# Kernel tuning notes

Measured on AMD Instinct MI355X. Metric: run time of the kernel, lower is better.

## Reference

```python
import jax, jax.numpy as jnp
import numpy as np

NUM_HEADS = 16
THETA = 10000.0
B, S, D = 2, 2048, 1024
D_K = D // NUM_HEADS


def setup_inputs() -> dict:
    key = jax.random.key(0)
    ks = jax.random.split(key, 5)
    s = 0.02
    return {
        "x": jax.random.normal(ks[0], (B, S, D), dtype=jnp.float32),
        "W_q": jax.random.normal(ks[1], (D, D), dtype=jnp.float32) * s,
        "W_k": jax.random.normal(ks[2], (D, D), dtype=jnp.float32) * s,
        "W_v": jax.random.normal(ks[3], (D, D), dtype=jnp.float32) * s,
        "W_o": jax.random.normal(ks[4], (D, D), dtype=jnp.float32) * s,
        "token_positions": jnp.arange(S, dtype=jnp.int32),
    }


def _rope(x, token_positions):
    # x: [..., seq, d_k]; equivalent to the block-diagonal 2x2 rotation matmul
    d2 = x.shape[-1] // 2
    inv_freq = THETA ** (-(2.0 * jnp.arange(d2, dtype=x.dtype)) / x.shape[-1])  # [d2]
    ang = token_positions.astype(x.dtype)[:, None] * inv_freq[None, :]  # [seq, d2]
    cos, sin = jnp.cos(ang), jnp.sin(ang)
    xp = x.reshape(x.shape[:-1] + (d2, 2))
    xe, xo = xp[..., 0], xp[..., 1]
    oe = cos * xe - sin * xo
    oo = sin * xe + cos * xo
    return jnp.stack([oe, oo], axis=-1).reshape(x.shape)


def reference(x, W_q, W_k, W_v, W_o, token_positions):
    seq = x.shape[-2]
    # QKV projections (weights stored as [out, in])
    Q = jnp.einsum('bsd,ed->bse', x, W_q)
    K = jnp.einsum('bsd,ed->bse', x, W_k)
    V = jnp.einsum('bsd,ed->bse', x, W_v)
    def split_heads(t):
        return t.reshape(t.shape[:-1] + (NUM_HEADS, D_K)).swapaxes(-3, -2)  # [b,h,s,dk]
    Q, K, V = split_heads(Q), split_heads(K), split_heads(V)
    Q = _rope(Q, token_positions)
    K = _rope(K, token_positions)
    scale = 1.0 / np.sqrt(D_K)
    scores = jnp.einsum('bhqd,bhkd->bhqk', Q, K) * scale
    causal = jnp.tril(jnp.ones((seq, seq), dtype=bool))
    scores = jnp.where(causal, scores, -jnp.inf)
    probs = jax.nn.softmax(scores, axis=-1)
    out = jnp.einsum('bhqk,bhkd->bhqd', probs, V)
    out = out.swapaxes(-3, -2).reshape(x.shape[:-1] + (D,))
    return jnp.einsum('bse,de->bsd', out, W_o)
```

## Files before the change

### kernel.cpp

```cpp
#include <hip/hip_runtime.h>
#include <hip/hip_bf16.h>
#include <math.h>

#define H_    16
#define DK_   64
#define Dm    1024
#define Bb    2
#define Ss    2048
#define Mrows 4096
#define QSCALE 0.1803368801f

typedef short s16x8 __attribute__((ext_vector_type(8)));
typedef float f32x4 __attribute__((ext_vector_type(4)));
typedef unsigned short u16;

__device__ __forceinline__ u16 f2b(float f) {
  __hip_bfloat16 h = __float2bfloat16(f);
  return *reinterpret_cast<u16*>(&h);
}
__device__ __forceinline__ float b2f(u16 u) {
  __hip_bfloat16 h;
  *reinterpret_cast<u16*>(&h) = u;
  return __bfloat162float(h);
}

#define GLDS(g, l)                                                             \
  __builtin_amdgcn_global_load_lds(                                            \
      (const __attribute__((address_space(1))) unsigned int*)(g),              \
      (__attribute__((address_space(3))) unsigned int*)(l), 16, 0, 0)

__device__ __forceinline__ int SW64(int row, int col) {
  return row * 64 + ((((col >> 3) ^ (row & 7) ^ (row >> 3)) & 7) << 3) + (col & 7);
}

__global__ __launch_bounds__(256) void k_castall(
    const float* __restrict__ x,  const float* __restrict__ Wq,
    const float* __restrict__ Wk, const float* __restrict__ Wv,
    const float* __restrict__ Wo,
    u16* __restrict__ xb,  u16* __restrict__ wqb, u16* __restrict__ wkb,
    u16* __restrict__ wvb, u16* __restrict__ wob) {
  int i = blockIdx.x * 256 + threadIdx.x;
  const float* s;
  u16* d;
  int off;
  if (i < 1048576) { s = x; d = xb; off = i; }
  else {
    int j = i - 1048576;
    int w = j >> 18;
    off = j & 262143;
    s = (w == 0) ? Wq : (w == 1) ? Wk : (w == 2) ? Wv : Wo;
    d = (w == 0) ? wqb : (w == 1) ? wkb : (w == 2) ? wvb : wob;
  }
  float4 v = reinterpret_cast<const float4*>(s)[off];
  ushort4 o;
  o.x = f2b(v.x); o.y = f2b(v.y); o.z = f2b(v.z); o.w = f2b(v.w);
  reinterpret_cast<ushort4*>(d)[off] = o;
}

__global__ __launch_bounds__(256) void k_ropetab(const int* __restrict__ pos,
                                                 float2* __restrict__ tab) {
  int t = blockIdx.x * 256 + threadIdx.x;
  int s = t >> 5, i = t & 31;
  float p = (float)pos[s];
  float ang = p * powf(10000.0f, -(float)i / 32.0f);
  tab[t] = make_float2(cosf(ang), sinf(ang));
}

__global__ __launch_bounds__(256) void k_rope2(u16* __restrict__ Q, u16* __restrict__ K,
                                               const float2* __restrict__ tab) {
  int t = blockIdx.x * 256 + threadIdx.x;
  int row = t >> 7;
  int c0 = (t & 127) << 3;
  int i0 = (c0 & 63) >> 1;
  const float2* tb = &tab[(row & (Ss - 1)) * 32 + i0];
  float2 cs[4];
#pragma unroll
  for (int j = 0; j < 4; ++j) cs[j] = tb[j];
  size_t off = (size_t)row * Dm + c0;
  s16x8 q = *reinterpret_cast<const s16x8*>(&Q[off]);
  s16x8 k = *reinterpret_cast<const s16x8*>(&K[off]);
  s16x8 qo, ko;
#pragma unroll
  for (int j = 0; j < 4; ++j) {
    float qe = b2f((u16)q[2 * j]), qd = b2f((u16)q[2 * j + 1]);
    qo[2 * j]     = (short)f2b((cs[j].x * qe - cs[j].y * qd) * QSCALE);
    qo[2 * j + 1] = (short)f2b((cs[j].y * qe + cs[j].x * qd) * QSCALE);
    float ke = b2f((u16)k[2 * j]), kd = b2f((u16)k[2 * j + 1]);
    ko[2 * j]     = (short)f2b(cs[j].x * ke - cs[j].y * kd);
    ko[2 * j + 1] = (short)f2b(cs[j].y * ke + cs[j].x * kd);
  }
  *reinterpret_cast<s16x8*>(&Q[off]) = qo;
  *reinterpret_cast<s16x8*>(&K[off]) = ko;
}

template <int BN>
__global__ __launch_bounds__(256) void k_gemm_bt(
    const u16* __restrict__ A,
    const u16* __restrict__ B0, const u16* __restrict__ B1, const u16* __restrict__ B2,
    u16* __restrict__ O0, u16* __restrict__ O1, u16* __restrict__ OVT,
    float* __restrict__ OF, int M, int N, int K, int f32out) {
  constexpr int NFR = BN / 32;
  __shared__ __align__(16) u16 lsA[128 * 32];
  __shared__ __align__(16) u16 lsB[BN * 32];
  const int tid = threadIdx.x, lane = tid & 63, wave = tid >> 6;
  const int quad = lane >> 4, l16 = lane & 15;
  const int wrow = wave >> 1, wcol = wave & 1;
  const int m0 = blockIdx.x * 128, n0 = blockIdx.y * BN;
  const int z = blockIdx.z;
  const u16* Bp = (z == 0) ? B0 : (z == 1) ? B1 : B2;
  u16* Op = (z == 0) ? O0 : O1;
  f32x4 acc[4][NFR] = {};

  for (int k0 = 0; k0 < K; k0 += 32) {
#pragma unroll
    for (int c = 0; c < 2; ++c) {
      int flat = (wave * 2 + c) * 512 + lane * 8;
      int row = flat >> 5;
      int gs = ((flat >> 3) & 3) ^ ((row >> 1) & 3);
      GLDS(A + (size_t)(m0 + row) * K + k0 + gs * 8, lsA + (wave * 2 + c) * 512);
    }
#pragma unroll
    for (int c = 0; c < BN / 64; ++c) {
      int cc = wave * (BN / 64) + c;
      int flat = cc * 512 + lane * 8;
      int row = flat >> 5;
      int gs = ((flat >> 3) & 3) ^ ((row >> 1) & 3);
      GLDS(Bp + (size_t)(n0 + row) * K + k0 + gs * 8, lsB + cc * 512);
    }
    __syncthreads();
    s16x8 af[4], bfr[NFR];
#pragma unroll
    for (int i = 0; i < 4; ++i) {
      int row = wrow * 64 + i * 16 + l16;
      af[i] = *reinterpret_cast<const s16x8*>(&lsA[row * 32 + ((quad ^ ((row >> 1) & 3)) << 3)]);
    }
#pragma unroll
    for (int i = 0; i < NFR; ++i) {
      int row = wcol * (BN / 2) + i * 16 + l16;
      bfr[i] = *reinterpret_cast<const s16x8*>(&lsB[row * 32 + ((quad ^ ((row >> 1) & 3)) << 3)]);
    }
#pragma unroll
    for (int mi = 0; mi < 4; ++mi)
#pragma unroll
      for (int ni = 0; ni < NFR; ++ni)
        acc[mi][ni] = __builtin_amdgcn_mfma_f32_16x16x32_bf16(af[mi], bfr[ni], acc[mi][ni], 0, 0, 0);
    __syncthreads();
  }

  if (!f32out && z == 2) {
#pragma unroll
    for (int mi = 0; mi < 4; ++mi)
#pragma unroll
      for (int ni = 0; ni < NFR; ++ni) {
        int row0 = m0 + wrow * 64 + mi * 16 + quad * 4;
        int col  = n0 + wcol * (BN / 2) + ni * 16 + l16;
        int bb = row0 >> 11, s0 = row0 & (Ss - 1);
        ushort4 pk;
        pk.x = f2b(acc[mi][ni][0]); pk.y = f2b(acc[mi][ni][1]);
        pk.z = f2b(acc[mi][ni][2]); pk.w = f2b(acc[mi][ni][3]);
        *reinterpret_cast<ushort4*>(&OVT[((size_t)bb * Dm + col) * Ss + s0]) = pk;
      }
    return;
  }
#pragma unroll
  for (int mi = 0; mi < 4; ++mi)
#pragma unroll
    for (int ni = 0; ni < NFR; ++ni)
#pragma unroll
      for (int r = 0; r < 4; ++r) {
        int row = m0 + wrow * 64 + mi * 16 + quad * 4 + r;
        int col = n0 + wcol * (BN / 2) + ni * 16 + l16;
        float v = acc[mi][ni][r];
        size_t idx = (size_t)row * N + col;
        if (f32out) OF[idx] = v;
        else        Op[idx] = f2b(v);
      }
}

__global__ __launch_bounds__(256) void k_flash(const u16* __restrict__ Q,
                                               const u16* __restrict__ K,
                                               const u16* __restrict__ VT,
                                               u16* __restrict__ O) {
  __shared__ __align__(16) u16 lsK[2][64 * 64];
  __shared__ __align__(16) u16 lsVT[2][64 * 64];
  __shared__ __align__(16) u16 lsP[4][32 * 64];
  const int tid = threadIdx.x, lane = tid & 63, wave = tid >> 6;
  const int quad = lane >> 4, l16 = lane & 15;
  const int bid = blockIdx.x;
  const int bh = bid & 31;
  const int h = bh & (H_ - 1), b = bh >> 4;
  const int g = bid >> 5, a = g & 7, bsel = g >> 3;
  const int qt = bsel ? (15 - a) : a;
  const int q0 = qt * 128;
  const int qbase = q0 + wave * 32;
  const int ktmax_w = (qbase + 31) >> 6;
  const int xorv = (l16 * 2) & 0xE;

  s16x8 qf[2][2];
#pragma unroll
  for (int s = 0; s < 2; ++s) {
    const size_t qoff = (size_t)(b * Ss + qbase + s * 16 + l16) * Dm + h * 64;
    qf[s][0] = *reinterpret_cast<const s16x8*>(&Q[qoff + quad * 8]);
    qf[s][1] = *reinterpret_cast<const s16x8*>(&Q[qoff + 32 + quad * 8]);
  }
  s16x8 ones;
#pragma unroll
  for (int j = 0; j < 8; ++j) ones[j] = (short)0x3F80;

  f32x4 ot[2][4] = {};
  f32x4 lAcc[2] = {};
  const int npairs = qt + 1;

  for (int pp = 0; pp < npairs; ++pp) {
    const int kt0 = pp * 2;
#pragma unroll
    for (int half = 0; half < 2; ++half) {
      const size_t kbase  = (size_t)(b * Ss + (kt0 + half) * 64) * Dm + h * 64;
      const size_t vtbase = ((size_t)b * Dm + h * 64) * Ss + (kt0 + half) * 64;
#pragma unroll
      for (int c = 0; c < 2; ++c) {
        int slot = (wave * 2 + c) * 64 + lane;
        int row = slot >> 3;
        int gg = ((slot & 7) ^ (row & 7) ^ (row >> 3)) & 7;
        GLDS(K  + kbase  + (size_t)row * Dm + gg * 8, lsK[half]  + (wave * 2 + c) * 512);
        GLDS(VT + vtbase + (size_t)row * Ss + gg * 8, lsVT[half] + (wave * 2 + c) * 512);
      }
    }
    __syncthreads();

#pragma unroll
    for (int half = 0; half < 2; ++half) {
      const int kt = kt0 + half;
      if (kt > ktmax_w) break;
      f32x4 st[2][4] = {};
#pragma unroll
      for (int kc = 0; kc < 2; ++kc)
#pragma unroll
        for (int ni = 0; ni < 4; ++ni) {
          s16x8 kf = *reinterpret_cast<const s16x8*>(
              &lsK[half][SW64(ni * 16 + l16, kc * 32 + quad * 8)]);
          st[0][ni] = __builtin_amdgcn_mfma_f32_16x16x32_bf16(kf, qf[0][kc], st[0][ni], 0, 0, 0);
          st[1][ni] = __builtin_amdgcn_mfma_f32_16x16x32_bf16(kf, qf[1][kc], st[1][ni], 0, 0, 0);
        }
      if (kt == ktmax_w) {
#pragma unroll
        for (int s = 0; s < 2; ++s) {
          int gq = qbase + s * 16 + l16;
#pragma unroll
          for (int ni = 0; ni < 4; ++ni)
#pragma unroll
            for (int r = 0; r < 4; ++r)
              if (kt * 64 + ni * 16 + quad * 4 + r > gq) st[s][ni][r] = -INFINITY;
        }
      }
#pragma unroll
      for (int s = 0; s < 2; ++s)
#pragma unroll
        for (int ni = 0; ni < 4; ++ni) {
          ushort4 pk;
          pk.x = f2b(exp2f(st[s][ni][0])); pk.y = f2b(exp2f(st[s][ni][1]));
          pk.z = f2b(exp2f(st[s][ni][2])); pk.w = f2b(exp2f(st[s][ni][3]));
          *reinterpret_cast<ushort4*>(
              &lsP[wave][(s * 16 + l16) * 64 + (((ni * 4 + quad) ^ xorv) << 2)]) = pk;
        }
#pragma unroll
      for (int kc = 0; kc < 2; ++kc) {
        s16x8 pf0 = *reinterpret_cast<const s16x8*>(
            &lsP[wave][l16 * 64 + (((kc * 8 + quad * 2) ^ xorv) << 2)]);
        s16x8 pf1 = *reinterpret_cast<const s16x8*>(
            &lsP[wave][(16 + l16) * 64 + (((kc * 8 + quad * 2) ^ xorv) << 2)]);
        lAcc[0] = __builtin_amdgcn_mfma_f32_16x16x32_bf16(ones, pf0, lAcc[0], 0, 0, 0);
        lAcc[1] = __builtin_amdgcn_mfma_f32_16x16x32_bf16(ones, pf1, lAcc[1], 0, 0, 0);
#pragma unroll
        for (int ni = 0; ni < 4; ++ni) {
          s16x8 vf = *reinterpret_cast<const s16x8*>(
              &lsVT[half][SW64(ni * 16 + l16, kc * 32 + quad * 8)]);
          ot[0][ni] = __builtin_amdgcn_mfma_f32_16x16x32_bf16(vf, pf0, ot[0][ni], 0, 0, 0);
          ot[1][ni] = __builtin_amdgcn_mfma_f32_16x16x32_bf16(vf, pf1, ot[1][ni], 0, 0, 0);
        }
      }
    }
    __syncthreads();
  }

#pragma unroll
  for (int s = 0; s < 2; ++s) {
    float inv = 1.0f / lAcc[s][0];
    const size_t obase = (size_t)(b * Ss + qbase + s * 16 + l16) * Dm + h * 64;
#pragma unroll
    for (int ni = 0; ni < 4; ++ni) {
      ushort4 pk;
      pk.x = f2b(ot[s][ni][0] * inv); pk.y = f2b(ot[s][ni][1] * inv);
      pk.z = f2b(ot[s][ni][2] * inv); pk.w = f2b(ot[s][ni][3] * inv);
      *reinterpret_cast<ushort4*>(&O[obase + ni * 16 + quad * 4]) = pk;
    }
  }
}

extern "C" void kernel_launch(void* const* d_in, const int* in_sizes, int n_in,
                              void* d_out, int out_size, void* d_ws, size_t ws_size,
                              hipStream_t stream) {
  const float* x  = (const float*)d_in[0];
  const float* Wq = (const float*)d_in[1];
  const float* Wk = (const float*)d_in[2];
  const float* Wv = (const float*)d_in[3];
  const float* Wo = (const float*)d_in[4];
  const int* pos  = (const int*)d_in[5];
  float* out = (float*)d_out;

  char* w = (char*)d_ws;
  u16* xb  = (u16*)w; w += (size_t)Mrows * Dm * 2;
  u16* wqb = (u16*)w; w += (size_t)Dm * Dm * 2;
  u16* wkb = (u16*)w; w += (size_t)Dm * Dm * 2;
  u16* wvb = (u16*)w; w += (size_t)Dm * Dm * 2;
  u16* wob = (u16*)w; w += (size_t)Dm * Dm * 2;
  u16* Qb  = (u16*)w; w += (size_t)Mrows * Dm * 2;
  u16* Kb  = (u16*)w; w += (size_t)Mrows * Dm * 2;
  u16* VTb = (u16*)w; w += (size_t)Mrows * Dm * 2;
  u16* Ab  = (u16*)w; w += (size_t)Mrows * Dm * 2;
  float2* tabf = (float2*)w; w += (size_t)Ss * 32 * sizeof(float2);

  k_castall<<<8192, 256, 0, stream>>>(x, Wq, Wk, Wv, Wo, xb, wqb, wkb, wvb, wob);
  k_ropetab<<<Ss * 32 / 256, 256, 0, stream>>>(pos, tabf);

  k_gemm_bt<128><<<dim3(32, 8, 3), 256, 0, stream>>>(xb, wqb, wkb, wvb,
                                                     Qb, Kb, VTb, nullptr,
                                                     Mrows, Dm, Dm, 0);
  k_rope2<<<Mrows * Dm / 8 / 256, 256, 0, stream>>>(Qb, Kb, tabf);
  k_flash<<<dim3(512), 256, 0, stream>>>(Qb, Kb, VTb, Ab);
  k_gemm_bt<64><<<dim3(32, 16, 1), 256, 0, stream>>>(Ab, wob, wob, wob,
                                                     nullptr, nullptr, nullptr, out,
                                                     Mrows, Dm, Dm, 1);
}
```

Before: 203.1 us.

## Double-buffer flash K/V loads, widen GEMM k-step, use fast exp2 and pack

The flash kernel moves from loading pairs of K/V tiles and then computing on them to a per-tile double-buffered pipeline, where the next tile is prefetched while the current one is processed, with one barrier per tile. The projection GEMM now steps K by 64 with the SW64 swizzle, halving the number of barriers and loop iterations at the cost of larger LDS tiles. Softmax exponentials use the raw hardware exp2 builtin, and bf16 packing uses a byte-perm that truncates instead of rounding, trading a little precision for fewer instructions. There is a possible race: with one barrier per tile, a fast wave can issue the prefetch into a buffer that slower waves may still be reading from the previous iteration.

Measured after the change: 202.1 us. No clear change (-0.5%).

```diff
diff --git a/kernel.cpp b/kernel.cpp
--- a/kernel.cpp
+++ b/kernel.cpp
@@ -13,6 +13,7 @@
 typedef short s16x8 __attribute__((ext_vector_type(8)));
 typedef float f32x4 __attribute__((ext_vector_type(4)));
 typedef unsigned short u16;
+typedef unsigned int u32;
 
 __device__ __forceinline__ u16 f2b(float f) {
   __hip_bfloat16 h = __float2bfloat16(f);
@@ -22,6 +23,9 @@
   __hip_bfloat16 h;
   *reinterpret_cast<u16*>(&h) = u;
   return __bfloat162float(h);
+}
+__device__ __forceinline__ u32 pkbf(float hi, float lo) {
+  return __builtin_amdgcn_perm(__float_as_uint(hi), __float_as_uint(lo), 0x07060302u);
 }
 
 #define GLDS(g, l)                                                             \
@@ -100,8 +104,8 @@
     u16* __restrict__ O0, u16* __restrict__ O1, u16* __restrict__ OVT,
     float* __restrict__ OF, int M, int N, int K, int f32out) {
   constexpr int NFR = BN / 32;
-  __shared__ __align__(16) u16 lsA[128 * 32];
-  __shared__ __align__(16) u16 lsB[BN * 32];
+  __shared__ __align__(16) u16 lsA[128 * 64];
+  __shared__ __align__(16) u16 lsB[BN * 64];
   const int tid = threadIdx.x, lane = tid & 63, wave = tid >> 6;
   const int quad = lane >> 4, l16 = lane & 15;
   const int wrow = wave >> 1, wcol = wave & 1;
@@ -111,39 +115,38 @@
   u16* Op = (z == 0) ? O0 : O1;
   f32x4 acc[4][NFR] = {};
 
-  for (int k0 = 0; k0 < K; k0 += 32) {
-#pragma unroll
-    for (int c = 0; c < 2; ++c) {
-      int flat = (wave * 2 + c) * 512 + lane * 8;
-      int row = flat >> 5;
-      int gs = ((flat >> 3) & 3) ^ ((row >> 1) & 3);
-      GLDS(A + (size_t)(m0 + row) * K + k0 + gs * 8, lsA + (wave * 2 + c) * 512);
-    }
-#pragma unroll
-    for (int c = 0; c < BN / 64; ++c) {
-      int cc = wave * (BN / 64) + c;
-      int flat = cc * 512 + lane * 8;
-      int row = flat >> 5;
-      int gs = ((flat >> 3) & 3) ^ ((row >> 1) & 3);
-      GLDS(Bp + (size_t)(n0 + row) * K + k0 + gs * 8, lsB + cc * 512);
+  for (int k0 = 0; k0 < K; k0 += 64) {
+#pragma unroll
+    for (int c = 0; c < 4; ++c) {
+      int slot = (wave * 4 + c) * 64 + lane;
+      int row = slot >> 3;
+      int gg = ((slot & 7) ^ (row & 7) ^ (row >> 3)) & 7;
+      GLDS(A + (size_t)(m0 + row) * K + k0 + gg * 8, lsA + (wave * 4 + c) * 512);
+    }
+#pragma unroll
+    for (int c = 0; c < BN / 32; ++c) {
+      int cc = wave * (BN / 32) + c;
+      int slot = cc * 64 + lane;
+      int row = slot >> 3;
+      int gg = ((slot & 7) ^ (row & 7) ^ (row >> 3)) & 7;
+      GLDS(Bp + (size_t)(n0 + row) * K + k0 + gg * 8, lsB + cc * 512);
     }
     __syncthreads();
-    s16x8 af[4], bfr[NFR];
-#pragma unroll
-    for (int i = 0; i < 4; ++i) {
-      int row = wrow * 64 + i * 16 + l16;
-      af[i] = *reinterpret_cast<const s16x8*>(&lsA[row * 32 + ((quad ^ ((row >> 1) & 3)) << 3)]);
-    }
-#pragma unroll
-    for (int i = 0; i < NFR; ++i) {
-      int row = wcol * (BN / 2) + i * 16 + l16;
-      bfr[i] = *reinterpret_cast<const s16x8*>(&lsB[row * 32 + ((quad ^ ((row >> 1) & 3)) << 3)]);
-    }
-#pragma unroll
-    for (int mi = 0; mi < 4; ++mi)
-#pragma unroll
-      for (int ni = 0; ni < NFR; ++ni)
-        acc[mi][ni] = __builtin_amdgcn_mfma_f32_16x16x32_bf16(af[mi], bfr[ni], acc[mi][ni], 0, 0, 0);
+#pragma unroll
+    for (int kc = 0; kc < 2; ++kc) {
+      s16x8 af[4], bfr[NFR];
+#pragma unroll
+      for (int i = 0; i < 4; ++i)
+        af[i] = *reinterpret_cast<const s16x8*>(&lsA[SW64(wrow * 64 + i * 16 + l16, kc * 32 + quad * 8)]);
+#pragma unroll
+      for (int i = 0; i < NFR; ++i)
+        bfr[i] = *reinterpret_cast<const s16x8*>(&lsB[SW64(wcol * (BN / 2) + i * 16 + l16, kc * 32 + quad * 8)]);
+#pragma unroll
+      for (int mi = 0; mi < 4; ++mi)
+#pragma unroll
+        for (int ni = 0; ni < NFR; ++ni)
+          acc[mi][ni] = __builtin_amdgcn_mfma_f32_16x16x32_bf16(af[mi], bfr[ni], acc[mi][ni], 0, 0, 0);
+    }
     __syncthreads();
   }
 
@@ -194,6 +197,7 @@
   const int q0 = qt * 128;
   const int qbase = q0 + wave * 32;
   const int ktmax_w = (qbase + 31) >> 6;
+  const int ktmax_b = 2 * qt + 1;
   const int xorv = (l16 * 2) & 0xE;
 
   s16x8 qf[2][2];
@@ -209,78 +213,78 @@
 
   f32x4 ot[2][4] = {};
   f32x4 lAcc[2] = {};
-  const int npairs = qt + 1;
-
-  for (int pp = 0; pp < npairs; ++pp) {
-    const int kt0 = pp * 2;
-#pragma unroll
-    for (int half = 0; half < 2; ++half) {
-      const size_t kbase  = (size_t)(b * Ss + (kt0 + half) * 64) * Dm + h * 64;
-      const size_t vtbase = ((size_t)b * Dm + h * 64) * Ss + (kt0 + half) * 64;
-#pragma unroll
-      for (int c = 0; c < 2; ++c) {
-        int slot = (wave * 2 + c) * 64 + lane;
-        int row = slot >> 3;
-        int gg = ((slot & 7) ^ (row & 7) ^ (row >> 3)) & 7;
-        GLDS(K  + kbase  + (size_t)row * Dm + gg * 8, lsK[half]  + (wave * 2 + c) * 512);
-        GLDS(VT + vtbase + (size_t)row * Ss + gg * 8, lsVT[half] + (wave * 2 + c) * 512);
-      }
-    }
+
+  auto stage = [&](int kt, int bi) {
+    const size_t kbase  = (size_t)(b * Ss + kt * 64) * Dm + h * 64;
+    const size_t vtbase = ((size_t)b * Dm + h * 64) * Ss + kt * 64;
+#pragma unroll
+    for (int c = 0; c < 2; ++c) {
+      int slot = (wave * 2 + c) * 64 + lane;
+      int row = slot >> 3;
+      int gg = ((slot & 7) ^ (row & 7) ^ (row >> 3)) & 7;
+      GLDS(K  + kbase  + (size_t)row * Dm + gg * 8, &lsK[bi][(wave * 2 + c) * 512]);
+      GLDS(VT + vtbase + (size_t)row * Ss + gg * 8, &lsVT[bi][(wave * 2 + c) * 512]);
+    }
+  };
+
+  stage(0, 0);
+  for (int kt = 0; kt <= ktmax_b; ++kt) {
     __syncthreads();
-
-#pragma unroll
-    for (int half = 0; half < 2; ++half) {
-      const int kt = kt0 + half;
-      if (kt > ktmax_w) break;
-      f32x4 st[2][4] = {};
-#pragma unroll
-      for (int kc = 0; kc < 2; ++kc)
-#pragma unroll
-        for (int ni = 0; ni < 4; ++ni) {
-          s16x8 kf = *reinterpret_cast<const s16x8*>(
-              &lsK[half][SW64(ni * 16 + l16, kc * 32 + quad * 8)]);
-          st[0][ni] = __builtin_amdgcn_mfma_f32_16x16x32_bf16(kf, qf[0][kc], st[0][ni], 0, 0, 0);
-          st[1][ni] = __builtin_amdgcn_mfma_f32_16x16x32_bf16(kf, qf[1][kc], st[1][ni], 0, 0, 0);
-        }
-      if (kt == ktmax_w) {
-#pragma unroll
-        for (int s = 0; s < 2; ++s) {
-          int gq = qbase + s * 16 + l16;
-#pragma unroll
-          for (int ni = 0; ni < 4; ++ni)
-#pragma unroll
-            for (int r = 0; r < 4; ++r)
-              if (kt * 64 + ni * 16 + quad * 4 + r > gq) st[s][ni][r] = -INFINITY;
-        }
-      }
-#pragma unroll
-      for (int s = 0; s < 2; ++s)
-#pragma unroll
-        for (int ni = 0; ni < 4; ++ni) {
-          ushort4 pk;
-          pk.x = f2b(exp2f(st[s][ni][0])); pk.y = f2b(exp2f(st[s][ni][1]));
-          pk.z = f2b(exp2f(st[s][ni][2])); pk.w = f2b(exp2f(st[s][ni][3]));
-          *reinterpret_cast<ushort4*>(
-              &lsP[wave][(s * 16 + l16) * 64 + (((ni * 4 + quad) ^ xorv) << 2)]) = pk;
-        }
-#pragma unroll
-      for (int kc = 0; kc < 2; ++kc) {
-        s16x8 pf0 = *reinterpret_cast<const s16x8*>(
-            &lsP[wave][l16 * 64 + (((kc * 8 + quad * 2) ^ xorv) << 2)]);
-        s16x8 pf1 = *reinterpret_cast<const s16x8*>(
-            &lsP[wave][(16 + l16) * 64 + (((kc * 8 + quad * 2) ^ xorv) << 2)]);
-        lAcc[0] = __builtin_amdgcn_mfma_f32_16x16x32_bf16(ones, pf0, lAcc[0], 0, 0, 0);
-        lAcc[1] = __builtin_amdgcn_mfma_f32_16x16x32_bf16(ones, pf1, lAcc[1], 0, 0, 0);
-#pragma unroll
-        for (int ni = 0; ni < 4; ++ni) {
-          s16x8 vf = *reinterpret_cast<const s16x8*>(
-              &lsVT[half][SW64(ni * 16 + l16, kc * 32 + quad * 8)]);
-          ot[0][ni] = __builtin_amdgcn_mfma_f32_16x16x32_bf16(vf, pf0, ot[0][ni], 0, 0, 0);
-          ot[1][ni] = __builtin_amdgcn_mfma_f32_16x16x32_bf16(vf, pf1, ot[1][ni], 0, 0, 0);
-        }
-      }
-    }
-    __syncthreads();
+    if (kt < ktmax_b) stage(kt + 1, (kt + 1) & 1);
+    if (kt > ktmax_w) continue;
+    const int bi = kt & 1;
+
+    f32x4 st[2][4] = {};
+#pragma unroll
+    for (int kc = 0; kc < 2; ++kc)
+#pragma unroll
+      for (int ni = 0; ni < 4; ++ni) {
+        s16x8 kf = *reinterpret_cast<const s16x8*>(
+            &lsK[bi][SW64(ni * 16 + l16, kc * 32 + quad * 8)]);
+        st[0][ni] = __builtin_amdgcn_mfma_f32_16x16x32_bf16(kf, qf[0][kc], st[0][ni], 0, 0, 0);
+        st[1][ni] = __builtin_amdgcn_mfma_f32_16x16x32_bf16(kf, qf[1][kc], st[1][ni], 0, 0, 0);
+      }
+    if (kt == ktmax_w) {
+#pragma unroll
+      for (int s = 0; s < 2; ++s) {
+        int gq = qbase + s * 16 + l16;
+#pragma unroll
+        for (int ni = 0; ni < 4; ++ni)
+#pragma unroll
+          for (int r = 0; r < 4; ++r)
+            if (kt * 64 + ni * 16 + quad * 4 + r > gq) st[s][ni][r] = -INFINITY;
+      }
+    }
+#pragma unroll
+    for (int s = 0; s < 2; ++s)
+#pragma unroll
+      for (int ni = 0; ni < 4; ++ni) {
+        float e0 = __builtin_amdgcn_exp2f(st[s][ni][0]);
+        float e1 = __builtin_amdgcn_exp2f(st[s][ni][1]);
+        float e2 = __builtin_amdgcn_exp2f(st[s][ni][2]);
+        float e3 = __builtin_amdgcn_exp2f(st[s][ni][3]);
+        uint2 pk;
+        pk.x = pkbf(e1, e0);
+        pk.y = pkbf(e3, e2);
+        *reinterpret_cast<uint2*>(
+            &lsP[wave][(s * 16 + l16) * 64 + (((ni * 4 + quad) ^ xorv) << 2)]) = pk;
+      }
+#pragma unroll
+    for (int kc = 0; kc < 2; ++kc) {
+      s16x8 pf0 = *reinterpret_cast<const s16x8*>(
+          &lsP[wave][l16 * 64 + (((kc * 8 + quad * 2) ^ xorv) << 2)]);
+      s16x8 pf1 = *reinterpret_cast<const s16x8*>(
+          &lsP[wave][(16 + l16) * 64 + (((kc * 8 + quad * 2) ^ xorv) << 2)]);
+      lAcc[0] = __builtin_amdgcn_mfma_f32_16x16x32_bf16(ones, pf0, lAcc[0], 0, 0, 0);
+      lAcc[1] = __builtin_amdgcn_mfma_f32_16x16x32_bf16(ones, pf1, lAcc[1], 0, 0, 0);
+#pragma unroll
+      for (int ni = 0; ni < 4; ++ni) {
+        s16x8 vf = *reinterpret_cast<const s16x8*>(
+            &lsVT[bi][SW64(ni * 16 + l16, kc * 32 + quad * 8)]);
+        ot[0][ni] = __builtin_amdgcn_mfma_f32_16x16x32_bf16(vf, pf0, ot[0][ni], 0, 0, 0);
+        ot[1][ni] = __builtin_amdgcn_mfma_f32_16x16x32_bf16(vf, pf1, ot[1][ni], 0, 0, 0);
+      }
+    }
   }
 
 #pragma unroll
```
